# Performance work log

Hardware: AMD Instinct MI355X
Metric: run time of the kernel (lower is better)

The kernel has to match this reference:

```python
import jax, jax.numpy as jnp
import numpy as np

B, NX, NY = 4, 16384, 16384
CX = CY = 256
CK = CV = 256
H = 8


def setup_inputs() -> dict:
    key = jax.random.key(0)
    ks = jax.random.split(key, 12)
    s = 0.02
    return {
        "x": jax.random.normal(ks[0], (B, NX, CX), jnp.float32),
        "y": jax.random.normal(ks[1], (B, NY, CY), jnp.float32),
        "x_pos_embed": jax.random.normal(ks[2], (B, NX, CX), jnp.float32),
        "y_pos_embed": jax.random.normal(ks[3], (B, NY, CY), jnp.float32),
        "Wq": jax.random.normal(ks[4], (CK, CX), jnp.float32) * s,
        "bq": jnp.zeros((CK,), jnp.float32),
        "Wk": jax.random.normal(ks[5], (CK, CY), jnp.float32) * s,
        "bk": jnp.zeros((CK,), jnp.float32),
        "Wv": jax.random.normal(ks[6], (CV, CY), jnp.float32) * s,
        "bv": jnp.zeros((CV,), jnp.float32),
        "Wr": jax.random.normal(ks[7], (CX, CV), jnp.float32) * s,
        "br": jnp.zeros((CX,), jnp.float32),
    }


def reference(x, y, x_pos_embed, y_pos_embed, Wq, bq, Wk, bk, Wv, bv, Wr, br):
    # Linear projections (nn.Linear: x @ W.T + b)
    q = (x + x_pos_embed) @ Wq.T + bq            # [B, Nx, Ck]
    k = (y + y_pos_embed) @ Wk.T + bk            # [B, Ny, Ck]
    v = y @ Wv.T + bv                            # [B, Ny, Cv]

    dk, dv = CK // H, CV // H
    # Split heads: [B, N, H, d] -> [B, H, N, d]
    q = q.reshape(B, NX, H, dk).transpose(0, 2, 1, 3)
    k = k.reshape(B, NY, H, dk).transpose(0, 2, 1, 3)
    v = v.reshape(B, NY, H, dv).transpose(0, 2, 1, 3)

    # key softmax over tokens (Ny); query softmax over per-head channels (dk)
    k = jax.nn.softmax(k, axis=2)                # [B, H, Ny, dk]
    q = jax.nn.softmax(q, axis=3)                # [B, H, Nx, dk]

    # context = softmax(K)^T V : [B, H, dk, dv]
    context = jnp.einsum('bhnk,bhnv->bhkv', k, v)
    # attended = Q context : [B, H, Nx, dv]
    attended = jnp.einsum('bhnk,bhkv->bhnv', q, context)

    # merge heads -> [B, Nx, Cv], reproject -> [B, Nx, Cx]
    agg = attended.transpose(0, 2, 1, 3).reshape(B, NX, CV)
    return agg @ Wr.T + br
```

## Files before the change

### kernel.cpp

```cpp
#include <hip/hip_runtime.h>


typedef float f32x4 __attribute__((ext_vector_type(4)));
typedef short s16x4 __attribute__((ext_vector_type(4)));
typedef short s16x8 __attribute__((ext_vector_type(8)));

#define MFMA16(A, B, C) __builtin_amdgcn_mfma_f32_16x16x32_bf16((A), (B), (C), 0, 0, 0)

__device__ __forceinline__ short f2bf(float f) {
    unsigned u = __builtin_bit_cast(unsigned, f);
    u = (u + 0x7FFFu + ((u >> 16) & 1u)) >> 16;
    return (short)u;
}
__device__ __forceinline__ float bf2f(short b) {
    unsigned u = ((unsigned)(unsigned short)b) << 16;
    return __builtin_bit_cast(float, u);
}

__global__ __launch_bounds__(256) void wcvt_kernel(
    const float* __restrict__ wq, const float* __restrict__ wk,
    const float* __restrict__ wv, const float* __restrict__ wr,
    short* __restrict__ wbf)
{
    int id = blockIdx.x * 256 + threadIdx.x;
    int m = id >> 13;
    int slot = id & 8191;
    int tile = slot >> 9;
    int ks   = (slot >> 6) & 7;
    int lane = slot & 63;
    int lrow = lane & 15, lgrp = lane >> 4;
    const float* src = (m == 0) ? wq : (m == 1) ? wk : (m == 2) ? wv : wr;
    const float* p = src + (size_t)(tile * 16 + lrow) * 256 + ks * 32 + lgrp * 8;
    f32x4 a = *(const f32x4*)p;
    f32x4 b = *(const f32x4*)(p + 4);
    s16x8 o;
    o[0]=f2bf(a[0]); o[1]=f2bf(a[1]); o[2]=f2bf(a[2]); o[3]=f2bf(a[3]);
    o[4]=f2bf(b[0]); o[5]=f2bf(b[1]); o[6]=f2bf(b[2]); o[7]=f2bf(b[3]);
    *(s16x8*)(wbf + (size_t)id * 8) = o;
}

__global__ __launch_bounds__(256) void kv_kernel(
    const float* __restrict__ y, const float* __restrict__ ypos,
    const short* __restrict__ wkp, const short* __restrict__ wvp,
    const float* __restrict__ bk, const float* __restrict__ bv,
    short* __restrict__ e_buf, short* __restrict__ v_buf)
{
    __shared__ short smem[32 * 512];
    short* ak = smem;
    short* av = smem + 32 * 256;
    const int row0 = blockIdx.x * 32;
    const int t = threadIdx.x;
    const int w = t >> 6, lane = t & 63;

    {
        f32x4 ly[8], lp[8];
        #pragma unroll
        for (int it = 0; it < 8; ++it) {
            int r = it * 4 + w;
            ly[it] = *(const f32x4*)(y    + (size_t)(row0 + r) * 256 + lane * 4);
            lp[it] = *(const f32x4*)(ypos + (size_t)(row0 + r) * 256 + lane * 4);
        }
        #pragma unroll
        for (int it = 0; it < 8; ++it) {
            int r = it * 4 + w;
            f32x4 a = ly[it];
            f32x4 k = a + lp[it];
            s16x4 ov, ok;
            ov[0]=f2bf(a[0]); ov[1]=f2bf(a[1]); ov[2]=f2bf(a[2]); ov[3]=f2bf(a[3]);
            ok[0]=f2bf(k[0]); ok[1]=f2bf(k[1]); ok[2]=f2bf(k[2]); ok[3]=f2bf(k[3]);
            int swz = ((lane >> 1) ^ (r & 7)) * 8 + (lane & 1) * 4;
            *(s16x4*)(av + r * 256 + swz) = ov;
            *(s16x4*)(ak + r * 256 + swz) = ok;
        }
    }
    __syncthreads();

    const int lrow = lane & 15, lgrp = lane >> 4;
    const bool is_k = (w < 2);
    const int colbase = (w & 1) * 128;
    const int tile0 = colbase >> 4;
    const short* WP = is_k ? wkp : wvp;
    const float* bp = is_k ? bk : bv;
    const short* A = is_k ? ak : av;

    float bias[8];
    #pragma unroll
    for (int nf = 0; nf < 8; ++nf) bias[nf] = bp[colbase + nf * 16 + lrow];

    s16x8 af[2][8];
    #pragma unroll
    for (int mf = 0; mf < 2; ++mf) {
        int rr = mf * 16 + lrow;
        #pragma unroll
        for (int ks = 0; ks < 8; ++ks) {
            int cs = ((ks * 4 + lgrp) ^ (rr & 7));
            af[mf][ks] = *(const s16x8*)(A + rr * 256 + cs * 8);
        }
    }
    __syncthreads();

    const short* wt = WP + lane * 8;
    s16x8 bf[2][8];
    #pragma unroll
    for (int k = 0; k < 8; ++k)
        bf[0][k] = *(const s16x8*)(wt + ((size_t)tile0 * 8 + k) * 512);

    #pragma unroll
    for (int nf = 0; nf < 8; ++nf) {
        const int cur = nf & 1, nxt = cur ^ 1;
        if (nf < 7) {
            #pragma unroll
            for (int k = 0; k < 8; ++k)
                bf[nxt][k] = *(const s16x8*)(wt + ((size_t)(tile0 + nf + 1) * 8 + k) * 512);
        }
        f32x4 a0 = (f32x4){0.f, 0.f, 0.f, 0.f};
        f32x4 a1 = (f32x4){0.f, 0.f, 0.f, 0.f};
        #pragma unroll
        for (int k = 0; k < 8; ++k) {
            a0 = MFMA16(af[0][k], bf[cur][k], a0);
            a1 = MFMA16(af[1][k], bf[cur][k], a1);
        }
        const int colp = (is_k ? 0 : 256) + colbase + nf * 16 + lrow;
        #pragma unroll
        for (int rr = 0; rr < 4; ++rr) {
            float v0 = a0[rr] + bias[nf];
            float v1 = a1[rr] + bias[nf];
            if (is_k) { v0 = __expf(v0); v1 = __expf(v1); }
            int lr0 = lgrp * 4 + rr;
            int lr1 = lr0 + 16;
            smem[lr0 * 512 + (((colp >> 3) ^ (lr0 & 7)) * 8) + (colp & 7)] = f2bf(v0);
            smem[lr1 * 512 + (((colp >> 3) ^ (lr1 & 7)) * 8) + (colp & 7)] = f2bf(v1);
        }
    }
    __syncthreads();

    {
        #pragma unroll
        for (int i = 0; i < 8; ++i) {
            int r = i * 4 + w;
            int grow = row0 + r;
            s16x8 val = *(const s16x8*)(smem + r * 512 + (lane ^ (r & 7)) * 8);
            if (lane < 32)
                *(s16x8*)(e_buf + (size_t)grow * 256 + lane * 8) = val;
            else
                *(s16x8*)(v_buf + (size_t)grow * 256 + (lane - 32) * 8) = val;
        }
    }
}

__global__ __launch_bounds__(256) void ctx_kernel(
    const short* __restrict__ e_buf, const short* __restrict__ v_buf,
    float* __restrict__ partials)
{
    __shared__ float se[128 * 32];
    __shared__ float sv[128 * 32];
    __shared__ float red[4 * 1056];
    const int cb = blockIdx.x, bh = blockIdx.y;
    const int b = bh >> 3, h = bh & 7;
    const int tok0 = b * 16384 + cb * 1024;
    const int t = threadIdx.x, w = t >> 6, lane = t & 63;
    const int ckb = (lane >> 3) * 4, cvb = (lane & 7) * 4;

    f32x4 acc[4];
    #pragma unroll
    for (int i = 0; i < 4; ++i) acc[i] = (f32x4){0.f, 0.f, 0.f, 0.f};
    f32x4 dn = (f32x4){0.f, 0.f, 0.f, 0.f};

    for (int it = 0; it < 8; ++it) {
        __syncthreads();
        #pragma unroll
        for (int s = 0; s < 2; ++s) {
            int id = t + s * 256;
            int rr = id >> 2, pp = id & 3;
            size_t g = (size_t)(tok0 + it * 128 + rr) * 256 + h * 32 + pp * 8;
            s16x8 ee = *(const s16x8*)(e_buf + g);
            s16x8 vv = *(const s16x8*)(v_buf + g);
            f32x4 e0 = {bf2f(ee[0]), bf2f(ee[1]), bf2f(ee[2]), bf2f(ee[3])};
            f32x4 e1 = {bf2f(ee[4]), bf2f(ee[5]), bf2f(ee[6]), bf2f(ee[7])};
            f32x4 v0 = {bf2f(vv[0]), bf2f(vv[1]), bf2f(vv[2]), bf2f(vv[3])};
            f32x4 v1 = {bf2f(vv[4]), bf2f(vv[5]), bf2f(vv[6]), bf2f(vv[7])};
            *(f32x4*)(se + rr * 32 + pp * 8)     = e0;
            *(f32x4*)(se + rr * 32 + pp * 8 + 4) = e1;
            *(f32x4*)(sv + rr * 32 + pp * 8)     = v0;
            *(f32x4*)(sv + rr * 32 + pp * 8 + 4) = v1;
        }
        __syncthreads();
        const int r0 = w * 32;
        #pragma unroll 8
        for (int rr = 0; rr < 32; ++rr) {
            f32x4 e4 = *(const f32x4*)(se + (r0 + rr) * 32 + ckb);
            f32x4 v4 = *(const f32x4*)(sv + (r0 + rr) * 32 + cvb);
            acc[0] += e4[0] * v4;
            acc[1] += e4[1] * v4;
            acc[2] += e4[2] * v4;
            acc[3] += e4[3] * v4;
            dn += e4;
        }
    }
    __syncthreads();
    #pragma unroll
    for (int i = 0; i < 4; ++i)
        *(f32x4*)(red + w * 1056 + (ckb + i) * 32 + cvb) = acc[i];
    if ((lane & 7) == 0)
        *(f32x4*)(red + w * 1056 + 1024 + ckb) = dn;
    __syncthreads();
    float* outp = partials + (size_t)(bh * 16 + cb) * 1056;
    for (int e = t; e < 1056; e += 256)
        outp[e] = red[e] + red[1056 + e] + red[2112 + e] + red[3168 + e];
}

__global__ __launch_bounds__(256) void ctx_reduce_kernel(
    const float* __restrict__ partials, short* __restrict__ ctxT)
{
    __shared__ float s[1056];
    const int bh = blockIdx.x, t = threadIdx.x;
    for (int e = t; e < 1056; e += 256) {
        float a = 0.f;
        for (int c = 0; c < 16; ++c) a += partials[(size_t)(bh * 16 + c) * 1056 + e];
        s[e] = a;
    }
    __syncthreads();
    for (int e = t; e < 1024; e += 256) {
        int ck = e >> 5, cv = e & 31;
        float val = s[e] / s[1024 + ck];
        ctxT[(size_t)bh * 1024 + cv * 32 + ck] = f2bf(val);
    }
}

__global__ __launch_bounds__(256) void qout_kernel(
    const float* __restrict__ x, const float* __restrict__ xpos,
    const short* __restrict__ wqp, const float* __restrict__ bq,
    const short* __restrict__ ctxT,
    const short* __restrict__ wrp, const float* __restrict__ br,
    float* __restrict__ out)
{
    __shared__ short alds[32 * 256];
    __shared__ short qlds[4][32 * 64];
    const int row0 = blockIdx.x * 32;
    const int b = row0 >> 14;
    const int t = threadIdx.x;
    const int w = t >> 6, lane = t & 63;

    {
        f32x4 lx[8], lp[8];
        #pragma unroll
        for (int it = 0; it < 8; ++it) {
            int r = it * 4 + w;
            lx[it] = *(const f32x4*)(x    + (size_t)(row0 + r) * 256 + lane * 4);
            lp[it] = *(const f32x4*)(xpos + (size_t)(row0 + r) * 256 + lane * 4);
        }
        #pragma unroll
        for (int it = 0; it < 8; ++it) {
            int r = it * 4 + w;
            f32x4 a = lx[it] + lp[it];
            s16x4 o;
            o[0]=f2bf(a[0]); o[1]=f2bf(a[1]); o[2]=f2bf(a[2]); o[3]=f2bf(a[3]);
            int swz = ((lane >> 1) ^ (r & 7)) * 8 + (lane & 1) * 4;
            *(s16x4*)(alds + r * 256 + swz) = o;
        }
    }
    __syncthreads();

    const int lrow = lane & 15, lgrp = lane >> 4;
    const int wc = w * 64;
    const int tile0 = wc >> 4;

    float biasq[4];
    #pragma unroll
    for (int nf = 0; nf < 4; ++nf) biasq[nf] = bq[wc + nf * 16 + lrow];

    f32x4 acc[2][4];
    #pragma unroll
    for (int mf = 0; mf < 2; ++mf)
        #pragma unroll
        for (int nf = 0; nf < 4; ++nf) acc[mf][nf] = (f32x4){0.f, 0.f, 0.f, 0.f};

    {
        const short* wq8 = wqp + lane * 8;
        s16x8 bfq[2][4];
        #pragma unroll
        for (int nf = 0; nf < 4; ++nf)
            bfq[0][nf] = *(const s16x8*)(wq8 + ((size_t)(tile0 + nf) * 8 + 0) * 512);
        #pragma unroll
        for (int ks = 0; ks < 8; ++ks) {
            const int cur = ks & 1, nxt = cur ^ 1;
            if (ks < 7) {
                #pragma unroll
                for (int nf = 0; nf < 4; ++nf)
                    bfq[nxt][nf] = *(const s16x8*)(wq8 + ((size_t)(tile0 + nf) * 8 + ks + 1) * 512);
            }
            s16x8 af[2];
            #pragma unroll
            for (int mf = 0; mf < 2; ++mf) {
                int rr = mf * 16 + lrow;
                int cs = (ks * 4 + lgrp) ^ (rr & 7);
                af[mf] = *(const s16x8*)(alds + rr * 256 + cs * 8);
            }
            #pragma unroll
            for (int nf = 0; nf < 4; ++nf) {
                acc[0][nf] = MFMA16(af[0], bfq[cur][nf], acc[0][nf]);
                acc[1][nf] = MFMA16(af[1], bfq[cur][nf], acc[1][nf]);
            }
        }
    }

    short* ql = (short*)qlds[w];
    #pragma unroll
    for (int mf = 0; mf < 2; ++mf) {
        f32x4 e[4];
        #pragma unroll
        for (int nf = 0; nf < 4; ++nf)
            #pragma unroll
            for (int rr = 0; rr < 4; ++rr)
                e[nf][rr] = __expf(acc[mf][nf][rr] + biasq[nf]);
        #pragma unroll
        for (int hl = 0; hl < 2; ++hl) {
            #pragma unroll
            for (int rr = 0; rr < 4; ++rr) {
                float s = e[hl * 2][rr] + e[hl * 2 + 1][rr];
                s += __shfl_xor(s, 1);
                s += __shfl_xor(s, 2);
                s += __shfl_xor(s, 4);
                s += __shfl_xor(s, 8);
                float rinv = 1.0f / s;
                int row = mf * 16 + lgrp * 4 + rr;
                #pragma unroll
                for (int n2 = 0; n2 < 2; ++n2) {
                    int colc = hl * 32 + n2 * 16 + lrow;
                    int cs = (colc >> 3) ^ (row & 7);
                    ql[row * 64 + cs * 8 + (colc & 7)] = f2bf(e[hl * 2 + n2][rr] * rinv);
                }
            }
        }
    }
    __syncthreads();

    f32x4 att[2][2][2];
    #pragma unroll
    for (int hl = 0; hl < 2; ++hl)
        #pragma unroll
        for (int mf = 0; mf < 2; ++mf)
            #pragma unroll
            for (int n2 = 0; n2 < 2; ++n2) att[hl][mf][n2] = (f32x4){0.f,0.f,0.f,0.f};

    #pragma unroll
    for (int hl = 0; hl < 2; ++hl) {
        const short* cbase = ctxT + (size_t)(b * 8 + w * 2 + hl) * 1024;
        s16x8 bctx[2];
        #pragma unroll
        for (int n2 = 0; n2 < 2; ++n2)
            bctx[n2] = *(const s16x8*)(cbase + (n2 * 16 + lrow) * 32 + lgrp * 8);
        #pragma unroll
        for (int mf = 0; mf < 2; ++mf) {
            int row = mf * 16 + lrow;
            int cs = (hl * 4 + lgrp) ^ (row & 7);
            s16x8 aq = *(const s16x8*)(ql + row * 64 + cs * 8);
            #pragma unroll
            for (int n2 = 0; n2 < 2; ++n2)
                att[hl][mf][n2] = MFMA16(aq, bctx[n2], att[hl][mf][n2]);
        }
    }

    #pragma unroll
    for (int hl = 0; hl < 2; ++hl)
      #pragma unroll
      for (int mf = 0; mf < 2; ++mf)
        #pragma unroll
        for (int n2 = 0; n2 < 2; ++n2)
          #pragma unroll
          for (int rr = 0; rr < 4; ++rr) {
              int row = mf * 16 + lgrp * 4 + rr;
              int col = wc + hl * 32 + n2 * 16 + lrow;
              int cs = (col >> 3) ^ (row & 7);
              alds[row * 256 + cs * 8 + (col & 7)] = f2bf(att[hl][mf][n2][rr]);
          }
    __syncthreads();

    float biasr[4];
    #pragma unroll
    for (int nf = 0; nf < 4; ++nf) biasr[nf] = br[wc + nf * 16 + lrow];

    f32x4 acc2[2][4];
    #pragma unroll
    for (int mf = 0; mf < 2; ++mf)
        #pragma unroll
        for (int nf = 0; nf < 4; ++nf) acc2[mf][nf] = (f32x4){0.f, 0.f, 0.f, 0.f};

    {
        const short* wr8 = wrp + lane * 8;
        s16x8 bfr[2][4];
        #pragma unroll
        for (int nf = 0; nf < 4; ++nf)
            bfr[0][nf] = *(const s16x8*)(wr8 + ((size_t)(tile0 + nf) * 8 + 0) * 512);
        #pragma unroll
        for (int ks = 0; ks < 8; ++ks) {
            const int cur = ks & 1, nxt = cur ^ 1;
            if (ks < 7) {
                #pragma unroll
                for (int nf = 0; nf < 4; ++nf)
                    bfr[nxt][nf] = *(const s16x8*)(wr8 + ((size_t)(tile0 + nf) * 8 + ks + 1) * 512);
            }
            s16x8 af[2];
            #pragma unroll
            for (int mf = 0; mf < 2; ++mf) {
                int rr = mf * 16 + lrow;
                int cs = (ks * 4 + lgrp) ^ (rr & 7);
                af[mf] = *(const s16x8*)(alds + rr * 256 + cs * 8);
            }
            #pragma unroll
            for (int nf = 0; nf < 4; ++nf) {
                acc2[0][nf] = MFMA16(af[0], bfr[cur][nf], acc2[0][nf]);
                acc2[1][nf] = MFMA16(af[1], bfr[cur][nf], acc2[1][nf]);
            }
        }
    }

    #pragma unroll
    for (int mf = 0; mf < 2; ++mf)
      #pragma unroll
      for (int nf = 0; nf < 4; ++nf)
        #pragma unroll
        for (int rr = 0; rr < 4; ++rr) {
            int grow = row0 + mf * 16 + lgrp * 4 + rr;
            out[(size_t)grow * 256 + wc + nf * 16 + lrow] = acc2[mf][nf][rr] + biasr[nf];
        }
}

extern "C" void kernel_launch(void* const* d_in, const int* in_sizes, int n_in,
                              void* d_out, int out_size, void* d_ws, size_t ws_size,
                              hipStream_t stream)
{
    const float* x    = (const float*)d_in[0];
    const float* y    = (const float*)d_in[1];
    const float* xpos = (const float*)d_in[2];
    const float* ypos = (const float*)d_in[3];
    const float* Wq   = (const float*)d_in[4];
    const float* bq   = (const float*)d_in[5];
    const float* Wk   = (const float*)d_in[6];
    const float* bk   = (const float*)d_in[7];
    const float* Wv   = (const float*)d_in[8];
    const float* bv   = (const float*)d_in[9];
    const float* Wr   = (const float*)d_in[10];
    const float* br   = (const float*)d_in[11];

    char*  ws    = (char*)d_ws;
    short* wbf   = (short*)(ws);
    short* ctxT  = (short*)(ws + 524288);
    float* parts = (float*)(ws + (1 << 20));
    short* e_buf = (short*)(ws + ((size_t)4 << 20));
    short* v_buf = e_buf + (size_t)65536 * 256;
    float* outp  = (float*)d_out;

    hipLaunchKernelGGL(wcvt_kernel, dim3(128), dim3(256), 0, stream,
                       Wq, Wk, Wv, Wr, wbf);
    hipLaunchKernelGGL(kv_kernel, dim3(2048), dim3(256), 0, stream,
                       y, ypos, wbf + 65536, wbf + 131072, bk, bv, e_buf, v_buf);
    hipLaunchKernelGGL(ctx_kernel, dim3(16, 32), dim3(256), 0, stream,
                       e_buf, v_buf, parts);
    hipLaunchKernelGGL(ctx_reduce_kernel, dim3(32), dim3(256), 0, stream,
                       parts, ctxT);
    hipLaunchKernelGGL(qout_kernel, dim3(2048), dim3(256), 0, stream,
                       x, xpos, wbf, bq, ctxT, wbf + 196608, br, outp);
}
```

Before: 168.6 us.

## Fuse K/V projection with context accumulation via MFMA and two-stage reduction

Merges the K/V projection kernel and the context kernel. Each block now projects 64 tokens in two 32-token halves and accumulates exp(K)^T V per head directly from shared memory with bf16 MFMA, instead of writing bf16 E/V buffers to global memory and reading them back. The softmax denominators come from shuffle reductions. Per-block partials (1024 blocks x 8 heads) are summed in two reduction kernels. This removes a large global write/read round trip of intermediate activations. The cost is more partial data to reduce, an extra launch, and gathering MFMA operands with scalar LDS loads.

```diff
diff --git a/kernel.cpp b/kernel.cpp
--- a/kernel.cpp
+++ b/kernel.cpp
@@ -39,184 +39,206 @@
     *(s16x8*)(wbf + (size_t)id * 8) = o;
 }
 
-__global__ __launch_bounds__(256) void kv_kernel(
+__global__ __launch_bounds__(256) void kvctx_kernel(
     const float* __restrict__ y, const float* __restrict__ ypos,
     const short* __restrict__ wkp, const short* __restrict__ wvp,
     const float* __restrict__ bk, const float* __restrict__ bv,
-    short* __restrict__ e_buf, short* __restrict__ v_buf)
+    float* __restrict__ partials)
 {
     __shared__ short smem[32 * 512];
     short* ak = smem;
     short* av = smem + 32 * 256;
-    const int row0 = blockIdx.x * 32;
     const int t = threadIdx.x;
     const int w = t >> 6, lane = t & 63;
-
-    {
-        f32x4 ly[8], lp[8];
-        #pragma unroll
-        for (int it = 0; it < 8; ++it) {
-            int r = it * 4 + w;
-            ly[it] = *(const f32x4*)(y    + (size_t)(row0 + r) * 256 + lane * 4);
-            lp[it] = *(const f32x4*)(ypos + (size_t)(row0 + r) * 256 + lane * 4);
-        }
-        #pragma unroll
-        for (int it = 0; it < 8; ++it) {
-            int r = it * 4 + w;
-            f32x4 a = ly[it];
-            f32x4 k = a + lp[it];
-            s16x4 ov, ok;
-            ov[0]=f2bf(a[0]); ov[1]=f2bf(a[1]); ov[2]=f2bf(a[2]); ov[3]=f2bf(a[3]);
-            ok[0]=f2bf(k[0]); ok[1]=f2bf(k[1]); ok[2]=f2bf(k[2]); ok[3]=f2bf(k[3]);
-            int swz = ((lane >> 1) ^ (r & 7)) * 8 + (lane & 1) * 4;
-            *(s16x4*)(av + r * 256 + swz) = ov;
-            *(s16x4*)(ak + r * 256 + swz) = ok;
-        }
-    }
-    __syncthreads();
-
     const int lrow = lane & 15, lgrp = lane >> 4;
     const bool is_k = (w < 2);
     const int colbase = (w & 1) * 128;
     const int tile0 = colbase >> 4;
     const short* WP = is_k ? wkp : wvp;
     const float* bp = is_k ? bk : bv;
-    const short* A = is_k ? ak : av;
+    const int row0 = blockIdx.x * 64;
 
     float bias[8];
     #pragma unroll
     for (int nf = 0; nf < 8; ++nf) bias[nf] = bp[colbase + nf * 16 + lrow];
 
-    s16x8 af[2][8];
-    #pragma unroll
-    for (int mf = 0; mf < 2; ++mf) {
-        int rr = mf * 16 + lrow;
-        #pragma unroll
-        for (int ks = 0; ks < 8; ++ks) {
-            int cs = ((ks * 4 + lgrp) ^ (rr & 7));
-            af[mf][ks] = *(const s16x8*)(A + rr * 256 + cs * 8);
-        }
-    }
-    __syncthreads();
-
-    const short* wt = WP + lane * 8;
-    s16x8 bf[2][8];
-    #pragma unroll
-    for (int k = 0; k < 8; ++k)
-        bf[0][k] = *(const s16x8*)(wt + ((size_t)tile0 * 8 + k) * 512);
-
-    #pragma unroll
-    for (int nf = 0; nf < 8; ++nf) {
-        const int cur = nf & 1, nxt = cur ^ 1;
-        if (nf < 7) {
-            #pragma unroll
-            for (int k = 0; k < 8; ++k)
-                bf[nxt][k] = *(const s16x8*)(wt + ((size_t)(tile0 + nf + 1) * 8 + k) * 512);
-        }
-        f32x4 a0 = (f32x4){0.f, 0.f, 0.f, 0.f};
-        f32x4 a1 = (f32x4){0.f, 0.f, 0.f, 0.f};
-        #pragma unroll
-        for (int k = 0; k < 8; ++k) {
-            a0 = MFMA16(af[0][k], bf[cur][k], a0);
-            a1 = MFMA16(af[1][k], bf[cur][k], a1);
-        }
-        const int colp = (is_k ? 0 : 256) + colbase + nf * 16 + lrow;
-        #pragma unroll
-        for (int rr = 0; rr < 4; ++rr) {
-            float v0 = a0[rr] + bias[nf];
-            float v1 = a1[rr] + bias[nf];
-            if (is_k) { v0 = __expf(v0); v1 = __expf(v1); }
-            int lr0 = lgrp * 4 + rr;
-            int lr1 = lr0 + 16;
-            smem[lr0 * 512 + (((colp >> 3) ^ (lr0 & 7)) * 8) + (colp & 7)] = f2bf(v0);
-            smem[lr1 * 512 + (((colp >> 3) ^ (lr1 & 7)) * 8) + (colp & 7)] = f2bf(v1);
-        }
-    }
-    __syncthreads();
-
-    {
-        #pragma unroll
-        for (int i = 0; i < 8; ++i) {
-            int r = i * 4 + w;
-            int grow = row0 + r;
-            s16x8 val = *(const s16x8*)(smem + r * 512 + (lane ^ (r & 7)) * 8);
-            if (lane < 32)
-                *(s16x8*)(e_buf + (size_t)grow * 256 + lane * 8) = val;
-            else
-                *(s16x8*)(v_buf + (size_t)grow * 256 + (lane - 32) * 8) = val;
-        }
-    }
-}
-
-__global__ __launch_bounds__(256) void ctx_kernel(
-    const short* __restrict__ e_buf, const short* __restrict__ v_buf,
-    float* __restrict__ partials)
-{
-    __shared__ float se[128 * 32];
-    __shared__ float sv[128 * 32];
-    __shared__ float red[4 * 1056];
-    const int cb = blockIdx.x, bh = blockIdx.y;
+    f32x4 cacc[2][2][2];
+    #pragma unroll
+    for (int a = 0; a < 2; ++a)
+      #pragma unroll
+      for (int b = 0; b < 2; ++b)
+        #pragma unroll
+        for (int c = 0; c < 2; ++c) cacc[a][b][c] = (f32x4){0.f,0.f,0.f,0.f};
+    float dacc[8];
+    #pragma unroll
+    for (int nf = 0; nf < 8; ++nf) dacc[nf] = 0.f;
+
+    f32x4 ly[8], lp[8];
+    #pragma unroll
+    for (int it = 0; it < 8; ++it) {
+        int r = it * 4 + w;
+        ly[it] = *(const f32x4*)(y    + (size_t)(row0 + r) * 256 + lane * 4);
+        lp[it] = *(const f32x4*)(ypos + (size_t)(row0 + r) * 256 + lane * 4);
+    }
+
+    for (int tt = 0; tt < 2; ++tt) {
+        {
+            #pragma unroll
+            for (int it = 0; it < 8; ++it) {
+                int r = it * 4 + w;
+                f32x4 a = ly[it];
+                f32x4 k = a + lp[it];
+                s16x4 ov, ok;
+                ov[0]=f2bf(a[0]); ov[1]=f2bf(a[1]); ov[2]=f2bf(a[2]); ov[3]=f2bf(a[3]);
+                ok[0]=f2bf(k[0]); ok[1]=f2bf(k[1]); ok[2]=f2bf(k[2]); ok[3]=f2bf(k[3]);
+                int swz = ((lane >> 1) ^ (r & 7)) * 8 + (lane & 1) * 4;
+                *(s16x4*)(av + r * 256 + swz) = ov;
+                *(s16x4*)(ak + r * 256 + swz) = ok;
+            }
+        }
+        __syncthreads();
+
+        s16x8 af[2][8];
+        {
+            const short* A = is_k ? ak : av;
+            #pragma unroll
+            for (int mf = 0; mf < 2; ++mf) {
+                int rr = mf * 16 + lrow;
+                #pragma unroll
+                for (int ks = 0; ks < 8; ++ks) {
+                    int cs = ((ks * 4 + lgrp) ^ (rr & 7));
+                    af[mf][ks] = *(const s16x8*)(A + rr * 256 + cs * 8);
+                }
+            }
+        }
+        if (tt == 0) {
+            #pragma unroll
+            for (int it = 0; it < 8; ++it) {
+                int r = it * 4 + w;
+                ly[it] = *(const f32x4*)(y    + (size_t)(row0 + 32 + r) * 256 + lane * 4);
+                lp[it] = *(const f32x4*)(ypos + (size_t)(row0 + 32 + r) * 256 + lane * 4);
+            }
+        }
+        __syncthreads();
+
+        #pragma unroll
+        for (int nf = 0; nf < 8; ++nf) {
+            const int tile = tile0 + nf;
+            const short* wt = WP + ((size_t)tile * 8) * 512 + lane * 8;
+            f32x4 a0 = (f32x4){0.f, 0.f, 0.f, 0.f};
+            f32x4 a1 = (f32x4){0.f, 0.f, 0.f, 0.f};
+            #pragma unroll
+            for (int kg = 0; kg < 2; ++kg) {
+                s16x8 bf[4];
+                #pragma unroll
+                for (int kk = 0; kk < 4; ++kk)
+                    bf[kk] = *(const s16x8*)(wt + (kg * 4 + kk) * 512);
+                #pragma unroll
+                for (int kk = 0; kk < 4; ++kk) {
+                    a0 = MFMA16(af[0][kg * 4 + kk], bf[kk], a0);
+                    a1 = MFMA16(af[1][kg * 4 + kk], bf[kk], a1);
+                }
+            }
+            const int colp = (is_k ? 0 : 256) + colbase + nf * 16 + lrow;
+            float ssum = 0.f;
+            #pragma unroll
+            for (int rr = 0; rr < 4; ++rr) {
+                float v0 = a0[rr] + bias[nf];
+                float v1 = a1[rr] + bias[nf];
+                if (is_k) { v0 = __expf(v0); v1 = __expf(v1); ssum += v0 + v1; }
+                int lr0 = lgrp * 4 + rr;
+                int lr1 = lr0 + 16;
+                smem[lr0 * 512 + (((colp >> 3) ^ (lr0 & 7)) * 8) + (colp & 7)] = f2bf(v0);
+                smem[lr1 * 512 + (((colp >> 3) ^ (lr1 & 7)) * 8) + (colp & 7)] = f2bf(v1);
+            }
+            if (is_k) {
+                ssum += __shfl_xor(ssum, 16);
+                ssum += __shfl_xor(ssum, 32);
+                dacc[nf] += ssum;
+            }
+        }
+        __syncthreads();
+
+        #pragma unroll
+        for (int hh = 0; hh < 2; ++hh) {
+            const int h = w * 2 + hh;
+            s16x8 ea[2], vb[2];
+            #pragma unroll
+            for (int mfc = 0; mfc < 2; ++mfc) {
+                int colp = h * 32 + mfc * 16 + lrow;
+                #pragma unroll
+                for (int j = 0; j < 8; ++j) {
+                    int tok = lgrp * 8 + j;
+                    ea[mfc][j] = smem[tok * 512 + (((colp >> 3) ^ (tok & 7)) * 8) + (colp & 7)];
+                }
+            }
+            #pragma unroll
+            for (int nfc = 0; nfc < 2; ++nfc) {
+                int colp = 256 + h * 32 + nfc * 16 + lrow;
+                #pragma unroll
+                for (int j = 0; j < 8; ++j) {
+                    int tok = lgrp * 8 + j;
+                    vb[nfc][j] = smem[tok * 512 + (((colp >> 3) ^ (tok & 7)) * 8) + (colp & 7)];
+                }
+            }
+            #pragma unroll
+            for (int mfc = 0; mfc < 2; ++mfc)
+                #pragma unroll
+                for (int nfc = 0; nfc < 2; ++nfc)
+                    cacc[hh][mfc][nfc] = MFMA16(ea[mfc], vb[nfc], cacc[hh][mfc][nfc]);
+        }
+        __syncthreads();
+    }
+
+    float* P = partials + (size_t)blockIdx.x * 8448;
+    #pragma unroll
+    for (int hh = 0; hh < 2; ++hh) {
+        const int h = w * 2 + hh;
+        #pragma unroll
+        for (int mfc = 0; mfc < 2; ++mfc)
+            #pragma unroll
+            for (int nfc = 0; nfc < 2; ++nfc)
+                #pragma unroll
+                for (int rr = 0; rr < 4; ++rr) {
+                    int ck = mfc * 16 + lgrp * 4 + rr;
+                    int cv = nfc * 16 + lrow;
+                    P[h * 1056 + ck * 32 + cv] = cacc[hh][mfc][nfc][rr];
+                }
+    }
+    if (is_k && lgrp == 0) {
+        #pragma unroll
+        for (int nf = 0; nf < 8; ++nf) {
+            int col = colbase + nf * 16 + lrow;
+            P[(col >> 5) * 1056 + 1024 + (col & 31)] = dacc[nf];
+        }
+    }
+}
+
+__global__ __launch_bounds__(256) void ctxred1_kernel(
+    const float* __restrict__ partials, float* __restrict__ inter)
+{
+    const int slab = blockIdx.x, bh = blockIdx.y;
     const int b = bh >> 3, h = bh & 7;
-    const int tok0 = b * 16384 + cb * 1024;
-    const int t = threadIdx.x, w = t >> 6, lane = t & 63;
-    const int ckb = (lane >> 3) * 4, cvb = (lane & 7) * 4;
-
-    f32x4 acc[4];
-    #pragma unroll
-    for (int i = 0; i < 4; ++i) acc[i] = (f32x4){0.f, 0.f, 0.f, 0.f};
-    f32x4 dn = (f32x4){0.f, 0.f, 0.f, 0.f};
-
-    for (int it = 0; it < 8; ++it) {
-        __syncthreads();
-        #pragma unroll
-        for (int s = 0; s < 2; ++s) {
-            int id = t + s * 256;
-            int rr = id >> 2, pp = id & 3;
-            size_t g = (size_t)(tok0 + it * 128 + rr) * 256 + h * 32 + pp * 8;
-            s16x8 ee = *(const s16x8*)(e_buf + g);
-            s16x8 vv = *(const s16x8*)(v_buf + g);
-            f32x4 e0 = {bf2f(ee[0]), bf2f(ee[1]), bf2f(ee[2]), bf2f(ee[3])};
-            f32x4 e1 = {bf2f(ee[4]), bf2f(ee[5]), bf2f(ee[6]), bf2f(ee[7])};
-            f32x4 v0 = {bf2f(vv[0]), bf2f(vv[1]), bf2f(vv[2]), bf2f(vv[3])};
-            f32x4 v1 = {bf2f(vv[4]), bf2f(vv[5]), bf2f(vv[6]), bf2f(vv[7])};
-            *(f32x4*)(se + rr * 32 + pp * 8)     = e0;
-            *(f32x4*)(se + rr * 32 + pp * 8 + 4) = e1;
-            *(f32x4*)(sv + rr * 32 + pp * 8)     = v0;
-            *(f32x4*)(sv + rr * 32 + pp * 8 + 4) = v1;
-        }
-        __syncthreads();
-        const int r0 = w * 32;
-        #pragma unroll 8
-        for (int rr = 0; rr < 32; ++rr) {
-            f32x4 e4 = *(const f32x4*)(se + (r0 + rr) * 32 + ckb);
-            f32x4 v4 = *(const f32x4*)(sv + (r0 + rr) * 32 + cvb);
-            acc[0] += e4[0] * v4;
-            acc[1] += e4[1] * v4;
-            acc[2] += e4[2] * v4;
-            acc[3] += e4[3] * v4;
-            dn += e4;
-        }
-    }
-    __syncthreads();
-    #pragma unroll
-    for (int i = 0; i < 4; ++i)
-        *(f32x4*)(red + w * 1056 + (ckb + i) * 32 + cvb) = acc[i];
-    if ((lane & 7) == 0)
-        *(f32x4*)(red + w * 1056 + 1024 + ckb) = dn;
-    __syncthreads();
-    float* outp = partials + (size_t)(bh * 16 + cb) * 1056;
-    for (int e = t; e < 1056; e += 256)
-        outp[e] = red[e] + red[1056 + e] + red[2112 + e] + red[3168 + e];
-}
-
-__global__ __launch_bounds__(256) void ctx_reduce_kernel(
-    const float* __restrict__ partials, short* __restrict__ ctxT)
+    const int t = threadIdx.x;
+    const float* base = partials + ((size_t)(b * 256 + slab * 32)) * 8448 + h * 1056;
+    float* obase = inter + (size_t)(bh * 8 + slab) * 1056;
+    for (int e = t; e < 1056; e += 256) {
+        float a = 0.f;
+        #pragma unroll 4
+        for (int i = 0; i < 32; ++i) a += base[(size_t)i * 8448 + e];
+        obase[e] = a;
+    }
+}
+
+__global__ __launch_bounds__(256) void ctxred2_kernel(
+    const float* __restrict__ inter, short* __restrict__ ctxT)
 {
     __shared__ float s[1056];
     const int bh = blockIdx.x, t = threadIdx.x;
     for (int e = t; e < 1056; e += 256) {
         float a = 0.f;
-        for (int c = 0; c < 16; ++c) a += partials[(size_t)(bh * 16 + c) * 1056 + e];
+        #pragma unroll
+        for (int i = 0; i < 8; ++i) a += inter[(size_t)(bh * 8 + i) * 1056 + e];
         s[e] = a;
     }
     __syncthreads();
@@ -446,19 +468,18 @@
     char*  ws    = (char*)d_ws;
     short* wbf   = (short*)(ws);
     short* ctxT  = (short*)(ws + 524288);
-    float* parts = (float*)(ws + (1 << 20));
-    short* e_buf = (short*)(ws + ((size_t)4 << 20));
-    short* v_buf = e_buf + (size_t)65536 * 256;
+    float* inter = (float*)(ws + (2u << 20));
+    float* parts = (float*)(ws + ((size_t)4 << 20));
     float* outp  = (float*)d_out;
 
     hipLaunchKernelGGL(wcvt_kernel, dim3(128), dim3(256), 0, stream,
                        Wq, Wk, Wv, Wr, wbf);
-    hipLaunchKernelGGL(kv_kernel, dim3(2048), dim3(256), 0, stream,
-                       y, ypos, wbf + 65536, wbf + 131072, bk, bv, e_buf, v_buf);
-    hipLaunchKernelGGL(ctx_kernel, dim3(16, 32), dim3(256), 0, stream,
-                       e_buf, v_buf, parts);
-    hipLaunchKernelGGL(ctx_reduce_kernel, dim3(32), dim3(256), 0, stream,
-                       parts, ctxT);
+    hipLaunchKernelGGL(kvctx_kernel, dim3(1024), dim3(256), 0, stream,
+                       y, ypos, wbf + 65536, wbf + 131072, bk, bv, parts);
+    hipLaunchKernelGGL(ctxred1_kernel, dim3(8, 32), dim3(256), 0, stream,
+                       parts, inter);
+    hipLaunchKernelGGL(ctxred2_kernel, dim3(32), dim3(256), 0, stream,
+                       inter, ctxT);
     hipLaunchKernelGGL(qout_kernel, dim3(2048), dim3(256), 0, stream,
                        x, xpos, wbf, bq, ctxT, wbf + 196608, br, outp);
 }
```

New measurement: 189.7 us. 12.5% more time.

## Make kv_kernel persistent over four row tiles with double-buffered global prefetch

Applied to the files above, without the earlier changes.

kv_kernel now handles 128 rows per block (four 32-row tiles) with a grid of 512 instead of 2048. Each block prefetches the next tile's y/ypos into registers while running MFMAs on the current tile, and stages the data through a double-buffered LDS region. Weight fragments are now reloaded per tile in groups of four instead of the old two-stage register prefetch, and barriers are replaced by a raw lgkmcnt wait plus s_barrier. The goal is to hide global load latency and amortise bias/setup per block. In exchange the kernel uses twice the LDS and fewer blocks, which may lower occupancy and parallelism, and it reloads weights for every tile.

```diff
diff --git a/kernel.cpp b/kernel.cpp
--- a/kernel.cpp
+++ b/kernel.cpp
@@ -15,6 +15,13 @@
 __device__ __forceinline__ float bf2f(short b) {
     unsigned u = ((unsigned)(unsigned short)b) << 16;
     return __builtin_bit_cast(float, u);
+}
+
+__device__ __forceinline__ void bar_lds() {
+    __builtin_amdgcn_sched_barrier(0);
+    asm volatile("s_waitcnt lgkmcnt(0)" ::: "memory");
+    __builtin_amdgcn_s_barrier();
+    __builtin_amdgcn_sched_barrier(0);
 }
 
 __global__ __launch_bounds__(256) void wcvt_kernel(
@@ -45,105 +52,128 @@
     const float* __restrict__ bk, const float* __restrict__ bv,
     short* __restrict__ e_buf, short* __restrict__ v_buf)
 {
-    __shared__ short smem[32 * 512];
-    short* ak = smem;
-    short* av = smem + 32 * 256;
-    const int row0 = blockIdx.x * 32;
+    __shared__ short smem[2][32 * 512];
     const int t = threadIdx.x;
     const int w = t >> 6, lane = t & 63;
-
-    {
-        f32x4 ly[8], lp[8];
-        #pragma unroll
-        for (int it = 0; it < 8; ++it) {
-            int r = it * 4 + w;
-            ly[it] = *(const f32x4*)(y    + (size_t)(row0 + r) * 256 + lane * 4);
-            lp[it] = *(const f32x4*)(ypos + (size_t)(row0 + r) * 256 + lane * 4);
-        }
-        #pragma unroll
-        for (int it = 0; it < 8; ++it) {
-            int r = it * 4 + w;
-            f32x4 a = ly[it];
-            f32x4 k = a + lp[it];
-            s16x4 ov, ok;
-            ov[0]=f2bf(a[0]); ov[1]=f2bf(a[1]); ov[2]=f2bf(a[2]); ov[3]=f2bf(a[3]);
-            ok[0]=f2bf(k[0]); ok[1]=f2bf(k[1]); ok[2]=f2bf(k[2]); ok[3]=f2bf(k[3]);
-            int swz = ((lane >> 1) ^ (r & 7)) * 8 + (lane & 1) * 4;
-            *(s16x4*)(av + r * 256 + swz) = ov;
-            *(s16x4*)(ak + r * 256 + swz) = ok;
-        }
-    }
-    __syncthreads();
-
     const int lrow = lane & 15, lgrp = lane >> 4;
     const bool is_k = (w < 2);
     const int colbase = (w & 1) * 128;
     const int tile0 = colbase >> 4;
     const short* WP = is_k ? wkp : wvp;
     const float* bp = is_k ? bk : bv;
-    const short* A = is_k ? ak : av;
+    const int base_row = blockIdx.x * 128;
 
     float bias[8];
     #pragma unroll
     for (int nf = 0; nf < 8; ++nf) bias[nf] = bp[colbase + nf * 16 + lrow];
 
-    s16x8 af[2][8];
-    #pragma unroll
-    for (int mf = 0; mf < 2; ++mf) {
-        int rr = mf * 16 + lrow;
-        #pragma unroll
-        for (int ks = 0; ks < 8; ++ks) {
-            int cs = ((ks * 4 + lgrp) ^ (rr & 7));
-            af[mf][ks] = *(const s16x8*)(A + rr * 256 + cs * 8);
-        }
-    }
-    __syncthreads();
-
-    const short* wt = WP + lane * 8;
-    s16x8 bf[2][8];
-    #pragma unroll
-    for (int k = 0; k < 8; ++k)
-        bf[0][k] = *(const s16x8*)(wt + ((size_t)tile0 * 8 + k) * 512);
-
-    #pragma unroll
-    for (int nf = 0; nf < 8; ++nf) {
-        const int cur = nf & 1, nxt = cur ^ 1;
-        if (nf < 7) {
-            #pragma unroll
-            for (int k = 0; k < 8; ++k)
-                bf[nxt][k] = *(const s16x8*)(wt + ((size_t)(tile0 + nf + 1) * 8 + k) * 512);
-        }
-        f32x4 a0 = (f32x4){0.f, 0.f, 0.f, 0.f};
-        f32x4 a1 = (f32x4){0.f, 0.f, 0.f, 0.f};
-        #pragma unroll
-        for (int k = 0; k < 8; ++k) {
-            a0 = MFMA16(af[0][k], bf[cur][k], a0);
-            a1 = MFMA16(af[1][k], bf[cur][k], a1);
-        }
-        const int colp = (is_k ? 0 : 256) + colbase + nf * 16 + lrow;
-        #pragma unroll
-        for (int rr = 0; rr < 4; ++rr) {
-            float v0 = a0[rr] + bias[nf];
-            float v1 = a1[rr] + bias[nf];
-            if (is_k) { v0 = __expf(v0); v1 = __expf(v1); }
-            int lr0 = lgrp * 4 + rr;
-            int lr1 = lr0 + 16;
-            smem[lr0 * 512 + (((colp >> 3) ^ (lr0 & 7)) * 8) + (colp & 7)] = f2bf(v0);
-            smem[lr1 * 512 + (((colp >> 3) ^ (lr1 & 7)) * 8) + (colp & 7)] = f2bf(v1);
-        }
-    }
-    __syncthreads();
-
-    {
-        #pragma unroll
-        for (int i = 0; i < 8; ++i) {
-            int r = i * 4 + w;
-            int grow = row0 + r;
-            s16x8 val = *(const s16x8*)(smem + r * 512 + (lane ^ (r & 7)) * 8);
-            if (lane < 32)
-                *(s16x8*)(e_buf + (size_t)grow * 256 + lane * 8) = val;
-            else
-                *(s16x8*)(v_buf + (size_t)grow * 256 + (lane - 32) * 8) = val;
+    f32x4 ly[8], lp[8];
+
+    #pragma unroll
+    for (int it = 0; it < 8; ++it) {
+        int r = it * 4 + w;
+        ly[it] = *(const f32x4*)(y    + (size_t)(base_row + r) * 256 + lane * 4);
+        lp[it] = *(const f32x4*)(ypos + (size_t)(base_row + r) * 256 + lane * 4);
+    }
+    #pragma unroll
+    for (int it = 0; it < 8; ++it) {
+        int r = it * 4 + w;
+        f32x4 a = ly[it];
+        f32x4 k = a + lp[it];
+        s16x4 ov, ok;
+        ov[0]=f2bf(a[0]); ov[1]=f2bf(a[1]); ov[2]=f2bf(a[2]); ov[3]=f2bf(a[3]);
+        ok[0]=f2bf(k[0]); ok[1]=f2bf(k[1]); ok[2]=f2bf(k[2]); ok[3]=f2bf(k[3]);
+        int swz = ((lane >> 1) ^ (r & 7)) * 8 + (lane & 1) * 4;
+        *(s16x4*)(&smem[0][0] + 8192 + r * 256 + swz) = ov;
+        *(s16x4*)(&smem[0][0] +        r * 256 + swz) = ok;
+    }
+    bar_lds();
+
+    for (int tt = 0; tt < 4; ++tt) {
+        const int buf = tt & 1;
+        short* SB = &smem[buf][0];
+
+        if (tt < 3) {
+            #pragma unroll
+            for (int it = 0; it < 8; ++it) {
+                int r = (tt + 1) * 32 + it * 4 + w;
+                ly[it] = *(const f32x4*)(y    + (size_t)(base_row + r) * 256 + lane * 4);
+                lp[it] = *(const f32x4*)(ypos + (size_t)(base_row + r) * 256 + lane * 4);
+            }
+        }
+
+        const short* A = SB + (is_k ? 0 : 8192);
+        s16x8 af[2][8];
+        #pragma unroll
+        for (int mf = 0; mf < 2; ++mf) {
+            int rr = mf * 16 + lrow;
+            #pragma unroll
+            for (int ks = 0; ks < 8; ++ks) {
+                int cs = ((ks * 4 + lgrp) ^ (rr & 7));
+                af[mf][ks] = *(const s16x8*)(A + rr * 256 + cs * 8);
+            }
+        }
+        bar_lds();
+
+        #pragma unroll
+        for (int nf = 0; nf < 8; ++nf) {
+            const int tile = tile0 + nf;
+            const short* wt = WP + ((size_t)tile * 8) * 512 + lane * 8;
+            f32x4 a0 = (f32x4){0.f, 0.f, 0.f, 0.f};
+            f32x4 a1 = (f32x4){0.f, 0.f, 0.f, 0.f};
+            #pragma unroll
+            for (int kg = 0; kg < 2; ++kg) {
+                s16x8 bf[4];
+                #pragma unroll
+                for (int kk = 0; kk < 4; ++kk)
+                    bf[kk] = *(const s16x8*)(wt + (kg * 4 + kk) * 512);
+                #pragma unroll
+                for (int kk = 0; kk < 4; ++kk) {
+                    a0 = MFMA16(af[0][kg * 4 + kk], bf[kk], a0);
+                    a1 = MFMA16(af[1][kg * 4 + kk], bf[kk], a1);
+                }
+            }
+            const int colp = (is_k ? 0 : 256) + colbase + nf * 16 + lrow;
+            #pragma unroll
+            for (int rr = 0; rr < 4; ++rr) {
+                float v0 = a0[rr] + bias[nf];
+                float v1 = a1[rr] + bias[nf];
+                if (is_k) { v0 = __expf(v0); v1 = __expf(v1); }
+                int lr0 = lgrp * 4 + rr;
+                int lr1 = lr0 + 16;
+                SB[lr0 * 512 + (((colp >> 3) ^ (lr0 & 7)) * 8) + (colp & 7)] = f2bf(v0);
+                SB[lr1 * 512 + (((colp >> 3) ^ (lr1 & 7)) * 8) + (colp & 7)] = f2bf(v1);
+            }
+        }
+
+        if (tt < 3) {
+            short* SN = &smem[buf ^ 1][0];
+            #pragma unroll
+            for (int it = 0; it < 8; ++it) {
+                int r = it * 4 + w;
+                f32x4 a = ly[it];
+                f32x4 k = a + lp[it];
+                s16x4 ov, ok;
+                ov[0]=f2bf(a[0]); ov[1]=f2bf(a[1]); ov[2]=f2bf(a[2]); ov[3]=f2bf(a[3]);
+                ok[0]=f2bf(k[0]); ok[1]=f2bf(k[1]); ok[2]=f2bf(k[2]); ok[3]=f2bf(k[3]);
+                int swz = ((lane >> 1) ^ (r & 7)) * 8 + (lane & 1) * 4;
+                *(s16x4*)(SN + 8192 + r * 256 + swz) = ov;
+                *(s16x4*)(SN +        r * 256 + swz) = ok;
+            }
+        }
+        bar_lds();
+
+        {
+            const int grow0 = base_row + tt * 32;
+            #pragma unroll
+            for (int i = 0; i < 8; ++i) {
+                int r = i * 4 + w;
+                s16x8 val = *(const s16x8*)(SB + r * 512 + ((lane ^ (r & 7)) << 3));
+                if (lane < 32)
+                    *(s16x8*)(e_buf + (size_t)(grow0 + r) * 256 + lane * 8) = val;
+                else
+                    *(s16x8*)(v_buf + (size_t)(grow0 + r) * 256 + (lane - 32) * 8) = val;
+            }
         }
     }
 }
@@ -453,7 +483,7 @@
 
     hipLaunchKernelGGL(wcvt_kernel, dim3(128), dim3(256), 0, stream,
                        Wq, Wk, Wv, Wr, wbf);
-    hipLaunchKernelGGL(kv_kernel, dim3(2048), dim3(256), 0, stream,
+    hipLaunchKernelGGL(kv_kernel, dim3(512), dim3(256), 0, stream,
                        y, ypos, wbf + 65536, wbf + 131072, bk, bv, e_buf, v_buf);
     hipLaunchKernelGGL(ctx_kernel, dim3(16, 32), dim3(256), 0, stream,
                        e_buf, v_buf, parts);
```

Result: slower. 194.0 us (+15.1%).
